# Kernel optimization log

Hardware: AMD Instinct MI355X
Metric: run time of the kernel (lower is better)

Reference implementation:

```python
import jax, jax.numpy as jnp
import numpy as np

E = 16   # num_experts
K = 4    # num_activated_experts
B, S, H, I = 4, 1024, 1024, 2048


def setup_inputs() -> dict:
    key = jax.random.key(0)
    k0, k1, k2, k3 = jax.random.split(key, 4)
    scale = 0.02
    return {
        "hidden_states": jax.random.normal(k0, (B, S, H), jnp.float32),
        "router_w": jax.random.normal(k1, (H, E), jnp.float32) * scale,
        "router_b": jnp.zeros((E,), jnp.float32),
        "w1": jax.random.normal(k2, (E, H, I), jnp.float32) * scale,
        "b1": jnp.zeros((E, I), jnp.float32),
        "w2": jax.random.normal(k3, (E, I, H), jnp.float32) * scale,
        "b2": jnp.zeros((E, H), jnp.float32),
    }


def reference(hidden_states, router_w, router_b, w1, b1, w2, b2):
    b, s, h = hidden_states.shape
    # router: softmax over experts, pick top-k, renormalize top-k weights
    logits = hidden_states @ router_w + router_b            # [B,S,E]
    probs = jax.nn.softmax(logits, axis=-1)
    topw, topi = jax.lax.top_k(probs, K)                    # [B,S,K]
    topw = topw / jnp.sum(topw, axis=-1, keepdims=True)
    # scatter top-k weights into dense per-expert combine weights [B,S,E]
    combine = jnp.sum(
        jax.nn.one_hot(topi, E, dtype=hidden_states.dtype) * topw[..., None],
        axis=2,
    )
    x = hidden_states.reshape(b * s, h)                     # [T,H]
    c = combine.reshape(b * s, E)                           # [T,E]

    def body(acc, expert):
        w1e, b1e, w2e, b2e, ce = expert
        hmid = jax.nn.gelu(x @ w1e + b1e, approximate=False)  # [T,I]
        return acc + (hmid @ w2e + b2e) * ce[:, None], None

    out, _ = jax.lax.scan(body, jnp.zeros_like(x), (w1, b1, w2, b2, c.T))
    return out.reshape(b, s, h)
```

## Files before the change

### kernel.cpp

```cpp
#include <hip/hip_runtime.h>

#define T_TOK 4096
#define H_DIM 1024
#define I_DIM 2048
#define E_NUM 16
#define K_TOP 4
#define BM 128
#define BK 32
#define MAX_TILES 144
#define PAD_PAIRS (MAX_TILES * BM)
#define RW_Q 4104

typedef __attribute__((ext_vector_type(8))) short s16x8;
typedef __attribute__((ext_vector_type(4))) float f32x4;
typedef __attribute__((ext_vector_type(4))) unsigned short u16x4;
typedef __attribute__((ext_vector_type(8))) unsigned short u16x8;

__device__ __forceinline__ unsigned short f2bf(float f) {
  unsigned u = __float_as_uint(f);
  u += 0x7fffu + ((u >> 16) & 1u);
  return (unsigned short)(u >> 16);
}

__device__ __forceinline__ void mfma_bf16(const s16x8& a, const s16x8& b, f32x4& c) {
  asm("v_mfma_f32_16x16x32_bf16 %0, %1, %2, %0" : "+v"(c) : "v"(a), "v"(b));
}

__device__ __forceinline__ void gld16(const void* g, void* l) {
  __builtin_amdgcn_global_load_lds(
      (const __attribute__((address_space(1))) unsigned int*)g,
      (__attribute__((address_space(3))) unsigned int*)l, 16, 0, 0);
}

__device__ __forceinline__ int tile_map(const int* counts, int ty, int* tsp) {
  int e = -1, acc = 0, base = 0;
#pragma unroll
  for (int ee = 0; ee < E_NUM; ++ee) {
    int tc = (counts[ee] + 127) >> 7;
    if (ty >= acc && ty < acc + tc) {
      e = ee;
      *tsp = base + ((ty - acc) << 7);
    }
    acc += tc;
    base += tc << 7;
  }
  return e;
}

__global__ __launch_bounds__(256) void router_kernel(
    const float* __restrict__ x, const float* __restrict__ rw,
    const float* __restrict__ rb, int* __restrict__ topi,
    float* __restrict__ topw, int* __restrict__ counts,
    unsigned short* __restrict__ xb) {
  __shared__ float rws[4 * RW_Q];
  const int tid = threadIdx.x;
  {
    const size_t base = (size_t)blockIdx.x * 16 * H_DIM;
#pragma unroll
    for (int it = 0; it < 8; ++it) {
      size_t idx = base + ((size_t)(it * 256 + tid)) * 8;
      f32x4 a = *(const f32x4*)(x + idx);
      f32x4 b = *(const f32x4*)(x + idx + 4);
      u16x8 o;
      o[0] = f2bf(a[0]); o[1] = f2bf(a[1]); o[2] = f2bf(a[2]); o[3] = f2bf(a[3]);
      o[4] = f2bf(b[0]); o[5] = f2bf(b[1]); o[6] = f2bf(b[2]); o[7] = f2bf(b[3]);
      *(u16x8*)(xb + idx) = o;
    }
  }
  for (int idx = tid * 4; idx < H_DIM * E_NUM; idx += 256 * 4) {
    f32x4 v = *(const f32x4*)(rw + idx);
    int h = idx >> 4, e0 = idx & 15;
    *(f32x4*)&rws[(h >> 8) * RW_Q + (h & 255) * 16 + e0] = v;
  }
  __syncthreads();
  const int w = tid >> 6, l = tid & 63;
  const int e = l & 15, q = l >> 4;
  const float rbe = rb[e];
  const float* ldsb = &rws[q * RW_Q + e];
#pragma unroll
  for (int i = 0; i < 4; ++i) {
    const int t = blockIdx.x * 16 + w * 4 + i;
    const float* xr = x + (size_t)t * H_DIM + (q << 8);
    float acc = 0.f;
#pragma unroll 8
    for (int hh = 0; hh < 256; hh += 4) {
      f32x4 xv = *(const f32x4*)(xr + hh);
      acc += xv[0] * ldsb[(hh + 0) * 16];
      acc += xv[1] * ldsb[(hh + 1) * 16];
      acc += xv[2] * ldsb[(hh + 2) * 16];
      acc += xv[3] * ldsb[(hh + 3) * 16];
    }
    acc += __shfl_xor(acc, 16);
    acc += __shfl_xor(acc, 32);
    float logit = acc + rbe;
    float m = logit;
    m = fmaxf(m, __shfl_xor(m, 1));
    m = fmaxf(m, __shfl_xor(m, 2));
    m = fmaxf(m, __shfl_xor(m, 4));
    m = fmaxf(m, __shfl_xor(m, 8));
    float ex = expf(logit - m);
    int rank = 0;
    const int b16 = l & 48;
#pragma unroll
    for (int j = 0; j < 16; ++j) {
      float vj = __shfl(ex, b16 + j);
      rank += (vj > ex) || (vj == ex && j < e);
    }
    float sel = (rank < K_TOP) ? ex : 0.f;
    float subs = sel;
    subs += __shfl_xor(subs, 1);
    subs += __shfl_xor(subs, 2);
    subs += __shfl_xor(subs, 4);
    subs += __shfl_xor(subs, 8);
    if (q == 0 && rank < K_TOP) {
      topi[t * K_TOP + rank] = e;
      topw[t * K_TOP + rank] = ex / subs;
      atomicAdd(&counts[e], 1);
    }
  }
}

__global__ __launch_bounds__(256) void scatter_kernel(
    const int* __restrict__ topi, const float* __restrict__ topw,
    const int* __restrict__ counts, int* __restrict__ cursor,
    int* __restrict__ pairTok, float* __restrict__ pairW,
    int* __restrict__ pairPos) {
  int padBase[E_NUM];
  int base = 0;
#pragma unroll
  for (int ee = 0; ee < E_NUM; ++ee) {
    padBase[ee] = base;
    base += ((counts[ee] + 127) >> 7) << 7;
  }
  int t = blockIdx.x * 256 + threadIdx.x;
  if (t >= T_TOK) return;
#pragma unroll
  for (int k = 0; k < K_TOP; ++k) {
    int e = topi[t * K_TOP + k];
    int pos = atomicAdd(&cursor[e], 1);
    int idx = padBase[e] + pos;
    pairTok[idx] = t;
    pairW[idx] = topw[t * K_TOP + k];
    pairPos[t * K_TOP + k] = idx;
  }
}

__device__ __forceinline__ void transpose_tile(const float* __restrict__ src,
                                               unsigned short* __restrict__ dst,
                                               int R, int C, int tx, int ty) {
  int r0 = ty * 64, c0 = tx * 64;
  __shared__ float tle[64][65];
  int rr = threadIdx.x >> 4, cc = (threadIdx.x & 15) * 4;
#pragma unroll
  for (int i = 0; i < 4; ++i) {
    f32x4 v = *(const f32x4*)(src + (size_t)(r0 + rr + 16 * i) * C + c0 + cc);
    tle[rr + 16 * i][cc + 0] = v[0];
    tle[rr + 16 * i][cc + 1] = v[1];
    tle[rr + 16 * i][cc + 2] = v[2];
    tle[rr + 16 * i][cc + 3] = v[3];
  }
  __syncthreads();
#pragma unroll
  for (int i = 0; i < 4; ++i) {
    int oc = c0 + rr + 16 * i;
    u16x4 o;
    o[0] = f2bf(tle[cc + 0][rr + 16 * i]);
    o[1] = f2bf(tle[cc + 1][rr + 16 * i]);
    o[2] = f2bf(tle[cc + 2][rr + 16 * i]);
    o[3] = f2bf(tle[cc + 3][rr + 16 * i]);
    *(u16x4*)(dst + (size_t)oc * R + r0 + cc) = o;
  }
}

__global__ __launch_bounds__(256) void transpose_kernel(
    const float* __restrict__ src, unsigned short* __restrict__ dst, int R,
    int C) {
  size_t es = (size_t)R * C;
  transpose_tile(src + es * blockIdx.z, dst + es * blockIdx.z, R, C,
                 blockIdx.x, blockIdx.y);
}

__global__ __launch_bounds__(256) void transpose2_kernel(
    const float* __restrict__ w1, const float* __restrict__ w2,
    unsigned short* __restrict__ wT1, unsigned short* __restrict__ wT2) {
  const int bid = blockIdx.x;
  const size_t es = (size_t)H_DIM * I_DIM;
  if (bid < 8192) {
    const int e = bid >> 9, tb = bid & 511;
    transpose_tile(w1 + es * e, wT1 + es * e, H_DIM, I_DIM, tb & 31, tb >> 5);
  } else {
    const int eb = bid - 8192;
    const int e = eb >> 9, tb = eb & 511;
    transpose_tile(w2 + es * e, wT2 + es * e, I_DIM, H_DIM, tb & 15, tb >> 4);
  }
}

__global__ __launch_bounds__(256, 4) void gemm1_kernel(
    const unsigned short* __restrict__ xb, const unsigned short* __restrict__ w1t,
    const float* __restrict__ b1, unsigned short* __restrict__ hmid,
    const int* __restrict__ pairTok, const int* __restrict__ counts) {
  const int bid = blockIdx.x;
  const int lin = (bid & 7) * 288 + (bid >> 3);
  const int tx = lin & 15, ty = lin >> 4;
  int tsp = 0;
  const int e = tile_map(counts, ty, &tsp);
  if (e < 0) return;
  const int n0 = tx * 128;
  __shared__ unsigned short As[2][BM * BK];
  __shared__ unsigned short Bs[2][BM * BK];
  const int tid = threadIdx.x, w = tid >> 6, l = tid & 63;
  const int rbase = w * 16 + (l >> 2);
  const int segp = (l & 3) ^ ((l >> 3) & 3);
  int tok0 = pairTok[tsp + rbase];
  if (tok0 < 0) tok0 = 0;
  int tok1 = pairTok[tsp + rbase + 64];
  if (tok1 < 0) tok1 = 0;
  const char* gA0 = (const char*)(xb + (size_t)tok0 * H_DIM) + segp * 16;
  const char* gA1 = (const char*)(xb + (size_t)tok1 * H_DIM) + segp * 16;
  const unsigned short* wbase = w1t + (size_t)e * I_DIM * H_DIM;
  const char* gB0 = (const char*)(wbase + (size_t)(n0 + rbase) * H_DIM) + segp * 16;
  const char* gB1 = (const char*)(wbase + (size_t)(n0 + rbase + 64) * H_DIM) + segp * 16;

  f32x4 acc[4][4];
#pragma unroll
  for (int m = 0; m < 4; ++m)
#pragma unroll
    for (int n = 0; n < 4; ++n) acc[m][n] = f32x4{0.f, 0.f, 0.f, 0.f};

  const int wr = w >> 1, wc = w & 1, lrow = l & 15, g = l >> 4;
  const int gs = g ^ ((l >> 1) & 3);
  const int NK = H_DIM / BK;

  gld16(gA0, &As[0][w * 512]);
  gld16(gA1, &As[0][2048 + w * 512]);
  gld16(gB0, &Bs[0][w * 512]);
  gld16(gB1, &Bs[0][2048 + w * 512]);

  for (int kt = 0; kt < NK; ++kt) {
    __syncthreads();
    if (kt + 1 < NK) {
      const int kb = (kt + 1) * 64;
      const int nb = (kt + 1) & 1;
      gld16(gA0 + kb, &As[nb][w * 512]);
      gld16(gA1 + kb, &As[nb][2048 + w * 512]);
      gld16(gB0 + kb, &Bs[nb][w * 512]);
      gld16(gB1 + kb, &Bs[nb][2048 + w * 512]);
    }
    const int cb = kt & 1;
    const s16x8* Ap = (const s16x8*)As[cb];
    const s16x8* Bp = (const s16x8*)Bs[cb];
    s16x8 av[4], bv[4];
#pragma unroll
    for (int m = 0; m < 4; ++m) av[m] = Ap[(wr * 64 + m * 16 + lrow) * 4 + gs];
#pragma unroll
    for (int n = 0; n < 4; ++n) bv[n] = Bp[(wc * 64 + n * 16 + lrow) * 4 + gs];
#pragma unroll
    for (int m = 0; m < 4; ++m)
#pragma unroll
      for (int n = 0; n < 4; ++n) mfma_bf16(av[m], bv[n], acc[m][n]);
  }

  const float* b1e = b1 + (size_t)e * I_DIM;
#pragma unroll
  for (int m = 0; m < 4; ++m) {
    const int rw0 = wr * 64 + m * 16 + g * 4;
#pragma unroll
    for (int n = 0; n < 4; ++n) {
      const int col = n0 + wc * 64 + n * 16 + lrow;
      const float bb = b1e[col];
      f32x4 v = acc[m][n];
#pragma unroll
      for (int j = 0; j < 4; ++j) {
        const int p = tsp + rw0 + j;
        float xv = v[j] + bb;
        float y = 0.7978845608028654f * (xv + 0.044715f * xv * xv * xv);
        float ey = __expf(2.f * y);
        float th = 1.f - 2.f / (ey + 1.f);
        float ge = 0.5f * xv * (1.f + th);
        hmid[(size_t)p * I_DIM + col] = f2bf(ge);
      }
    }
  }
}

__global__ __launch_bounds__(256, 4) void gemm2_kernel(
    const unsigned short* __restrict__ hmid,
    const unsigned short* __restrict__ w2t, const float* __restrict__ b2,
    float* __restrict__ out, unsigned short* __restrict__ poA,
    unsigned short* __restrict__ poB, const int* __restrict__ pairTok,
    const float* __restrict__ pairW, const int* __restrict__ counts, int mode) {
  const int bid = blockIdx.x;
  const int nchunk = (mode == 2) ? 288 : 144;
  const int lin = (bid & 7) * nchunk + (bid >> 3);
  const int kh = (mode == 2) ? (lin & 1) : 0;
  const int tx = (mode == 2) ? ((lin >> 1) & 7) : (lin & 7);
  const int ty = (mode == 2) ? (lin >> 4) : (lin >> 3);
  int tsp = 0;
  const int e = tile_map(counts, ty, &tsp);
  if (e < 0) return;
  const int n0 = tx * 128;
  __shared__ unsigned short As[2][BM * BK];
  __shared__ unsigned short Bs[2][BM * BK];
  const int tid = threadIdx.x, w = tid >> 6, l = tid & 63;
  const int rbase = w * 16 + (l >> 2);
  const int segp = (l & 3) ^ ((l >> 3) & 3);
  const size_t koff = (size_t)kh * 2048;
  const char* gA0 =
      (const char*)(hmid + (size_t)(tsp + rbase) * I_DIM) + segp * 16 + koff;
  const char* gA1 =
      (const char*)(hmid + (size_t)(tsp + rbase + 64) * I_DIM) + segp * 16 + koff;
  const unsigned short* wbase = w2t + (size_t)e * H_DIM * I_DIM;
  const char* gB0 =
      (const char*)(wbase + (size_t)(n0 + rbase) * I_DIM) + segp * 16 + koff;
  const char* gB1 =
      (const char*)(wbase + (size_t)(n0 + rbase + 64) * I_DIM) + segp * 16 + koff;

  f32x4 acc[4][4];
#pragma unroll
  for (int m = 0; m < 4; ++m)
#pragma unroll
    for (int n = 0; n < 4; ++n) acc[m][n] = f32x4{0.f, 0.f, 0.f, 0.f};

  const int wr = w >> 1, wc = w & 1, lrow = l & 15, g = l >> 4;
  const int gs = g ^ ((l >> 1) & 3);
  const int NK = (mode == 2) ? 32 : 64;

  gld16(gA0, &As[0][w * 512]);
  gld16(gA1, &As[0][2048 + w * 512]);
  gld16(gB0, &Bs[0][w * 512]);
  gld16(gB1, &Bs[0][2048 + w * 512]);

  for (int kt = 0; kt < NK; ++kt) {
    __syncthreads();
    if (kt + 1 < NK) {
      const int kb = (kt + 1) * 64;
      const int nb = (kt + 1) & 1;
      gld16(gA0 + kb, &As[nb][w * 512]);
      gld16(gA1 + kb, &As[nb][2048 + w * 512]);
      gld16(gB0 + kb, &Bs[nb][w * 512]);
      gld16(gB1 + kb, &Bs[nb][2048 + w * 512]);
    }
    const int cb = kt & 1;
    const s16x8* Ap = (const s16x8*)As[cb];
    const s16x8* Bp = (const s16x8*)Bs[cb];
    s16x8 av[4], bv[4];
#pragma unroll
    for (int m = 0; m < 4; ++m) av[m] = Ap[(wr * 64 + m * 16 + lrow) * 4 + gs];
#pragma unroll
    for (int n = 0; n < 4; ++n) bv[n] = Bp[(wc * 64 + n * 16 + lrow) * 4 + gs];
#pragma unroll
    for (int m = 0; m < 4; ++m)
#pragma unroll
      for (int n = 0; n < 4; ++n) mfma_bf16(av[m], bv[n], acc[m][n]);
  }

  if (mode >= 1) {
    unsigned short* po = (kh == 0) ? poA : poB;
#pragma unroll
    for (int m = 0; m < 4; ++m) {
      const int rw0 = wr * 64 + m * 16 + g * 4;
#pragma unroll
      for (int n = 0; n < 4; ++n) {
        const int col = n0 + wc * 64 + n * 16 + lrow;
        f32x4 v = acc[m][n];
#pragma unroll
        for (int j = 0; j < 4; ++j)
          po[(size_t)(tsp + rw0 + j) * H_DIM + col] = f2bf(v[j]);
      }
    }
  } else {
    const float* b2e = b2 + (size_t)e * H_DIM;
#pragma unroll
    for (int m = 0; m < 4; ++m) {
      const int rw0 = wr * 64 + m * 16 + g * 4;
#pragma unroll
      for (int j = 0; j < 4; ++j) {
        const int p = tsp + rw0 + j;
        const int tok = pairTok[p];
        if (tok < 0) continue;
        const float pw = pairW[p];
        float* orow = out + (size_t)tok * H_DIM;
#pragma unroll
        for (int n = 0; n < 4; ++n) {
          const int col = n0 + wc * 64 + n * 16 + lrow;
          float val = (acc[m][n][j] + b2e[col]) * pw;
          atomicAdd(orow + col, val);
        }
      }
    }
  }
}

__global__ __launch_bounds__(256) void combine_kernel(
    const unsigned short* __restrict__ poA, const unsigned short* __restrict__ poB,
    const int* __restrict__ pairPos, const int* __restrict__ topi,
    const float* __restrict__ topw, const float* __restrict__ b2,
    float* __restrict__ out, int nbuf) {
  const int t = blockIdx.x * 2 + (threadIdx.x >> 7);
  const int c0 = (threadIdx.x & 127) * 8;
  float o[8];
#pragma unroll
  for (int j = 0; j < 8; ++j) o[j] = 0.f;
#pragma unroll
  for (int k = 0; k < K_TOP; ++k) {
    const int e = topi[t * K_TOP + k];
    const float pw = topw[t * K_TOP + k];
    const int pos = pairPos[t * K_TOP + k];
    u16x8 va = *(const u16x8*)(poA + (size_t)pos * H_DIM + c0);
    u16x8 vb;
    if (nbuf == 2) vb = *(const u16x8*)(poB + (size_t)pos * H_DIM + c0);
    const float* b2r = b2 + (size_t)e * H_DIM + c0;
#pragma unroll
    for (int j = 0; j < 8; ++j) {
      float hv = __uint_as_float((unsigned)va[j] << 16);
      if (nbuf == 2) hv += __uint_as_float((unsigned)vb[j] << 16);
      o[j] += pw * (hv + b2r[j]);
    }
  }
  float* orow = out + (size_t)t * H_DIM + c0;
  *(f32x4*)orow = f32x4{o[0], o[1], o[2], o[3]};
  *(f32x4*)(orow + 4) = f32x4{o[4], o[5], o[6], o[7]};
}

extern "C" void kernel_launch(void* const* d_in, const int* in_sizes, int n_in,
                              void* d_out, int out_size, void* d_ws,
                              size_t ws_size, hipStream_t stream) {
  const float* x = (const float*)d_in[0];
  const float* rw = (const float*)d_in[1];
  const float* rb = (const float*)d_in[2];
  const float* w1 = (const float*)d_in[3];
  const float* b1 = (const float*)d_in[4];
  const float* w2 = (const float*)d_in[5];
  const float* b2 = (const float*)d_in[6];
  float* out = (float*)d_out;
  char* ws = (char*)d_ws;

  const size_t xbSz = (size_t)T_TOK * H_DIM * 2;
  const size_t poSz = (size_t)PAD_PAIRS * H_DIM * 2;
  const size_t wtSz = (size_t)E_NUM * H_DIM * I_DIM * 2;
  const size_t hmSz = (size_t)PAD_PAIRS * I_DIM * 2;
  const size_t smallSz = (size_t)T_TOK * K_TOP * 4 * 3
                         + (size_t)PAD_PAIRS * 4 * 2
                         + 128;
  const size_t need3 = poSz * 2 + wtSz * 2 + hmSz + smallSz;
  const size_t need2 = poSz * 2 + wtSz + hmSz + smallSz;
  const size_t need1 = poSz + wtSz + hmSz + smallSz;
  const size_t need0 = xbSz + wtSz + hmSz + smallSz;
  int mode;
  if (ws_size >= need3) mode = 3;
  else if (ws_size >= need2) mode = 2;
  else if (ws_size >= need1) mode = 1;
  else if (ws_size >= need0) mode = 0;
  else return;

  size_t off = 0;
  unsigned short* xb = (unsigned short*)(ws + off);
  unsigned short* poA = (unsigned short*)(ws + off);
  off += (mode >= 1) ? poSz : xbSz;
  unsigned short* poB = (unsigned short*)(ws + off);
  if (mode >= 2) off += poSz;
  unsigned short* wT1 = (unsigned short*)(ws + off);
  off += wtSz;
  unsigned short* wT2 = wT1;
  if (mode == 3) { wT2 = (unsigned short*)(ws + off); off += wtSz; }
  unsigned short* hmid = (unsigned short*)(ws + off);
  off += hmSz;
  int* topi = (int*)(ws + off);      off += (size_t)T_TOK * K_TOP * 4;
  float* topw = (float*)(ws + off);  off += (size_t)T_TOK * K_TOP * 4;
  int* pairPos = (int*)(ws + off);   off += (size_t)T_TOK * K_TOP * 4;
  int* pairTok = (int*)(ws + off);   off += (size_t)PAD_PAIRS * 4;
  float* pairW = (float*)(ws + off); off += (size_t)PAD_PAIRS * 4;
  int* counts = (int*)(ws + off);    off += 64;
  int* cursor = (int*)(ws + off);    off += 64;

  const int gmode = (mode >= 2) ? 2 : mode;

  hipMemsetAsync(counts, 0, 128, stream);
  hipMemsetAsync(pairTok, 0xFF, (size_t)PAD_PAIRS * 4, stream);
  if (gmode == 0) hipMemsetAsync(out, 0, (size_t)T_TOK * H_DIM * 4, stream);

  router_kernel<<<T_TOK / 16, 256, 0, stream>>>(x, rw, rb, topi, topw, counts,
                                                xb);
  scatter_kernel<<<T_TOK / 256, 256, 0, stream>>>(topi, topw, counts, cursor,
                                                  pairTok, pairW, pairPos);
  if (mode == 3) {
    transpose2_kernel<<<16384, 256, 0, stream>>>(w1, w2, wT1, wT2);
    gemm1_kernel<<<16 * MAX_TILES, 256, 0, stream>>>(xb, wT1, b1, hmid, pairTok,
                                                     counts);
  } else {
    transpose_kernel<<<dim3(I_DIM / 64, H_DIM / 64, E_NUM), 256, 0, stream>>>(
        w1, wT1, H_DIM, I_DIM);
    gemm1_kernel<<<16 * MAX_TILES, 256, 0, stream>>>(xb, wT1, b1, hmid, pairTok,
                                                     counts);
    transpose_kernel<<<dim3(H_DIM / 64, I_DIM / 64, E_NUM), 256, 0, stream>>>(
        w2, wT2, I_DIM, H_DIM);
  }
  gemm2_kernel<<<(gmode == 2 ? 16 : 8) * MAX_TILES, 256, 0, stream>>>(
      hmid, wT2, b2, out, poA, poB, pairTok, pairW, counts, gmode);
  if (gmode >= 1)
    combine_kernel<<<T_TOK / 2, 256, 0, stream>>>(poA, poB, pairPos, topi, topw,
                                                  b2, out, gmode);
}
```

Baseline: 417.4 us.

## Triple-buffer gemm2 LDS pipeline and fill pad tokens in scatter kernel

The gemm2 main loop moves from a double-buffered LDS scheme to a three-stage ring. Loads for stage t+2 are issued while stage t is computed, with explicit vmcnt waits, raw s_barrier, hand-written ds_read_b128 with immediate offsets, and setprio around the MFMA block. Occupancy drops from 4 to 3 blocks per CU to make room for the larger LDS footprint. Separately, the pairTok memset is removed and the scatter kernel writes -1 only into the padded slots, saving one memset launch.

```diff
diff --git a/kernel.cpp b/kernel.cpp
--- a/kernel.cpp
+++ b/kernel.cpp
@@ -15,6 +15,9 @@
 typedef __attribute__((ext_vector_type(4))) float f32x4;
 typedef __attribute__((ext_vector_type(4))) unsigned short u16x4;
 typedef __attribute__((ext_vector_type(8))) unsigned short u16x8;
+
+#define DSR(dst, addr, off) \
+  asm volatile("ds_read_b128 %0, %1 offset:" #off : "=v"(dst) : "v"(addr))
 
 __device__ __forceinline__ unsigned short f2bf(float f) {
   unsigned u = __float_as_uint(f);
@@ -132,8 +135,7 @@
     padBase[ee] = base;
     base += ((counts[ee] + 127) >> 7) << 7;
   }
-  int t = blockIdx.x * 256 + threadIdx.x;
-  if (t >= T_TOK) return;
+  const int t = blockIdx.x * 256 + threadIdx.x;
 #pragma unroll
   for (int k = 0; k < K_TOP; ++k) {
     int e = topi[t * K_TOP + k];
@@ -142,6 +144,13 @@
     pairTok[idx] = t;
     pairW[idx] = topw[t * K_TOP + k];
     pairPos[t * K_TOP + k] = idx;
+  }
+#pragma unroll
+  for (int ee = 0; ee < E_NUM; ++ee) {
+    int c = counts[ee];
+    int padded = ((c + 127) >> 7) << 7;
+    int o = c + t;
+    if (o < padded) pairTok[padBase[ee] + o] = -1;
   }
 }
 
@@ -283,12 +292,13 @@
   }
 }
 
-__global__ __launch_bounds__(256, 4) void gemm2_kernel(
+__global__ __launch_bounds__(256, 3) void gemm2_kernel(
     const unsigned short* __restrict__ hmid,
     const unsigned short* __restrict__ w2t, const float* __restrict__ b2,
     float* __restrict__ out, unsigned short* __restrict__ poA,
     unsigned short* __restrict__ poB, const int* __restrict__ pairTok,
     const float* __restrict__ pairW, const int* __restrict__ counts, int mode) {
+  __shared__ char LDS[49152];
   const int bid = blockIdx.x;
   const int nchunk = (mode == 2) ? 288 : 144;
   const int lin = (bid & 7) * nchunk + (bid >> 3);
@@ -299,8 +309,6 @@
   const int e = tile_map(counts, ty, &tsp);
   if (e < 0) return;
   const int n0 = tx * 128;
-  __shared__ unsigned short As[2][BM * BK];
-  __shared__ unsigned short Bs[2][BM * BK];
   const int tid = threadIdx.x, w = tid >> 6, l = tid & 63;
   const int rbase = w * 16 + (l >> 2);
   const int segp = (l & 3) ^ ((l >> 3) & 3);
@@ -325,34 +333,52 @@
   const int gs = g ^ ((l >> 1) & 3);
   const int NK = (mode == 2) ? 32 : 64;
 
-  gld16(gA0, &As[0][w * 512]);
-  gld16(gA1, &As[0][2048 + w * 512]);
-  gld16(gB0, &Bs[0][w * 512]);
-  gld16(gB1, &Bs[0][2048 + w * 512]);
-
-  for (int kt = 0; kt < NK; ++kt) {
-    __syncthreads();
-    if (kt + 1 < NK) {
-      const int kb = (kt + 1) * 64;
-      const int nb = (kt + 1) & 1;
-      gld16(gA0 + kb, &As[nb][w * 512]);
-      gld16(gA1 + kb, &As[nb][2048 + w * 512]);
-      gld16(gB0 + kb, &Bs[nb][w * 512]);
-      gld16(gB1 + kb, &Bs[nb][2048 + w * 512]);
-    }
-    const int cb = kt & 1;
-    const s16x8* Ap = (const s16x8*)As[cb];
-    const s16x8* Bp = (const s16x8*)Bs[cb];
+  char* dA = LDS + w * 1024;
+  char* dB = LDS + 24576 + w * 1024;
+  const unsigned ldsb = (unsigned)(uintptr_t)&LDS[0];
+  const unsigned aRd = ldsb + (unsigned)((wr * 64 + lrow) * 64 + gs * 16);
+  const unsigned bRd = ldsb + 24576u + (unsigned)((wc * 64 + lrow) * 64 + gs * 16);
+
+  asm volatile("s_waitcnt vmcnt(0)" ::: "memory");
+  gld16(gA0, dA);        gld16(gA1, dA + 4096);
+  gld16(gB0, dB);        gld16(gB1, dB + 4096);
+  gld16(gA0 + 64, dA + 8192);  gld16(gA1 + 64, dA + 8192 + 4096);
+  gld16(gB0 + 64, dB + 8192);  gld16(gB1 + 64, dB + 8192 + 4096);
+
+  int srd = 0, sst = 2;
+  for (int t = 0; t < NK; ++t) {
+    if (t + 1 < NK)
+      asm volatile("s_waitcnt vmcnt(4)" ::: "memory");
+    else
+      asm volatile("s_waitcnt vmcnt(0)" ::: "memory");
+    asm volatile("s_barrier" ::: "memory");
+    const int tau = t + 2;
+    if (tau < NK) {
+      const size_t kb = (size_t)tau * 64;
+      char* da = dA + sst * 8192;
+      char* db = dB + sst * 8192;
+      gld16(gA0 + kb, da);  gld16(gA1 + kb, da + 4096);
+      gld16(gB0 + kb, db);  gld16(gB1 + kb, db + 4096);
+    }
+    const unsigned so = (unsigned)(srd * 8192);
+    const unsigned aS = aRd + so, bS = bRd + so;
     s16x8 av[4], bv[4];
-#pragma unroll
-    for (int m = 0; m < 4; ++m) av[m] = Ap[(wr * 64 + m * 16 + lrow) * 4 + gs];
-#pragma unroll
-    for (int n = 0; n < 4; ++n) bv[n] = Bp[(wc * 64 + n * 16 + lrow) * 4 + gs];
+    DSR(bv[0], bS, 0);    DSR(bv[1], bS, 1024);
+    DSR(bv[2], bS, 2048); DSR(bv[3], bS, 3072);
+    DSR(av[0], aS, 0);    DSR(av[1], aS, 1024);
+    DSR(av[2], aS, 2048); DSR(av[3], aS, 3072);
+    asm volatile("s_waitcnt lgkmcnt(0)" ::: "memory");
+    __builtin_amdgcn_sched_barrier(0);
+    __builtin_amdgcn_s_setprio(1);
 #pragma unroll
     for (int m = 0; m < 4; ++m)
 #pragma unroll
       for (int n = 0; n < 4; ++n) mfma_bf16(av[m], bv[n], acc[m][n]);
-  }
+    __builtin_amdgcn_s_setprio(0);
+    srd = (srd == 2) ? 0 : srd + 1;
+    sst = (sst == 2) ? 0 : sst + 1;
+  }
+  __builtin_amdgcn_sched_barrier(0);
 
   if (mode >= 1) {
     unsigned short* po = (kh == 0) ? poA : poB;
@@ -440,8 +466,7 @@
   const size_t wtSz = (size_t)E_NUM * H_DIM * I_DIM * 2;
   const size_t hmSz = (size_t)PAD_PAIRS * I_DIM * 2;
   const size_t smallSz = (size_t)T_TOK * K_TOP * 4 * 3
-                         + (size_t)PAD_PAIRS * 4 * 2
-                         + 128;
+                         + (size_t)PAD_PAIRS * 4 * 2 + 128;
   const size_t need3 = poSz * 2 + wtSz * 2 + hmSz + smallSz;
   const size_t need2 = poSz * 2 + wtSz + hmSz + smallSz;
   const size_t need1 = poSz + wtSz + hmSz + smallSz;
@@ -476,7 +501,6 @@
   const int gmode = (mode >= 2) ? 2 : mode;
 
   hipMemsetAsync(counts, 0, 128, stream);
-  hipMemsetAsync(pairTok, 0xFF, (size_t)PAD_PAIRS * 4, stream);
   if (gmode == 0) hipMemsetAsync(out, 0, (size_t)T_TOK * H_DIM * 4, stream);
 
   router_kernel<<<T_TOK / 16, 256, 0, stream>>>(x, rw, rb, topi, topw, counts,
```

After: 412.5 us. About the same (-1.2%).
